# Kernel tuning notes

Measured on AMD Instinct MI355X. Metric: run time of the kernel, lower is better.

The kernel has to match this reference:

```python
import jax, jax.numpy as jnp
import numpy as np

NUM_HEADS = 8
SCALES = (1, 2, 4)
EPS = 1e-06


def _linear_attention(q, k, v, scale):
    # q: [B,h,Nq,d], k,v: [B,h,N,d]; all float32 (matches .float() in torch)
    q = jax.nn.elu(q * scale) + 1.0
    k = jax.nn.elu(k * scale) + 1.0
    kv = jnp.einsum('bhnd,bhne->bhde', k, v)          # [B,h,d,d]
    o = jnp.einsum('bhnd,bhde->bhne', q, kv)          # [B,h,Nq,d]
    k_sum = k.sum(axis=2)                              # [B,h,d]
    norm = jnp.einsum('bhnd,bhd->bhn', q, k_sum)[..., None]
    norm = jnp.maximum(norm, EPS)
    return o / norm


def setup_inputs() -> dict:
    key = jax.random.key(0)
    k1, k2, k3 = jax.random.split(key, 3)
    B, C, H, W = 4, 256, 128, 128
    x = jax.random.normal(k1, (B, C, H, W), dtype=jnp.float32)
    W_qkv = jax.random.normal(k2, (3 * C, C), dtype=jnp.float32) * 0.02
    W_proj = jax.random.normal(k3, (C, C), dtype=jnp.float32) * 0.02
    scale_weights = jnp.ones((len(SCALES),), dtype=jnp.float32) / len(SCALES)
    return {'x': x, 'W_qkv': W_qkv, 'W_proj': W_proj, 'scale_weights': scale_weights}


def reference(x, W_qkv, W_proj, scale_weights):
    B, C, H, W = x.shape
    h = NUM_HEADS
    d = C // h
    N = H * W
    scale = d ** (-0.5)

    # 1x1 conv == channel matmul
    qkv = jnp.einsum('bchw,oc->bohw', x, W_qkv)        # [B,3C,H,W]
    qkv = qkv.reshape(B, 3, h, d, N)
    qkv = jnp.transpose(qkv, (1, 0, 2, 4, 3))          # [3,B,h,N,d]
    q, k, v = qkv[0], qkv[1], qkv[2]

    sw = jax.nn.softmax(scale_weights)
    out = sw[0] * _linear_attention(q, k, v, scale)    # [B,h,N,d]

    for i, s in enumerate(SCALES[1:], 1):
        pH, pW = max(1, H // s), max(1, W // s)
        # adaptive avg pool with divisible sizes == block mean
        qg = q.reshape(B, h, H, W, d)
        qp = qg.reshape(B, h, pH, s, pW, s, d).mean(axis=(3, 5))  # [B,h,pH,pW,d]
        qp = qp.reshape(B, h, pH * pW, d)
        ao = _linear_attention(qp, k, v, scale).reshape(B, h, pH, pW, d)
        # bilinear, align_corners=False (half-pixel) == jax 'linear'
        ao = jax.image.resize(ao, (B, h, H, W, d), method='linear')
        out = out + sw[i] * ao.reshape(B, h, N, d)

    # [B,h,N,d] -> [B,N,C] -> [B,C,H,W]
    out = jnp.transpose(out, (0, 2, 1, 3)).reshape(B, N, C)
    out = jnp.transpose(out, (0, 2, 1)).reshape(B, C, H, W)
    out = jnp.einsum('bchw,oc->bohw', out, W_proj)
    return out
```

## Files before the change

### kernel.cpp

```cpp
#include <hip/hip_runtime.h>
#include <cstdint>
#include <cstddef>

#define GN 16384
#define QK_SCALE 0.17677669529663687f

typedef __attribute__((ext_vector_type(8))) __bf16 bf16x8;
typedef __attribute__((ext_vector_type(4))) float f32x4;
typedef __attribute__((ext_vector_type(8))) unsigned short us8;
typedef __attribute__((ext_vector_type(4))) unsigned short us4;

__device__ __forceinline__ float qk_act(float z) {
  return z > 0.0f ? z + 1.0f : __expf(z);
}

__device__ __forceinline__ unsigned short f2bf_rn(float v) {
  union { float f; unsigned u; } a; a.f = v;
  unsigned u = a.u;
  unsigned r = u + 0x7fffu + ((u >> 16) & 1u);
  return (unsigned short)(r >> 16);
}
__device__ __forceinline__ float bf2f(unsigned short h) {
  union { unsigned u; float f; } a; a.u = ((unsigned)h) << 16; return a.f;
}

#define GLLDS(SRC, DST) __builtin_amdgcn_global_load_lds( \
    (const __attribute__((address_space(1))) void*)(SRC), \
    (__attribute__((address_space(3))) void*)(DST), 16, 0, 0)

__global__ __launch_bounds__(256) void split_w(
    const float* __restrict__ in, unsigned short* __restrict__ h,
    unsigned short* __restrict__ l, int n4)
{
  int i = blockIdx.x * 256 + threadIdx.x;
  if (i >= n4) return;
  float4 v = ((const float4*)in)[i];
  us4 vh, vl;
  vh[0] = f2bf_rn(v.x); vl[0] = f2bf_rn(v.x - bf2f(vh[0]));
  vh[1] = f2bf_rn(v.y); vl[1] = f2bf_rn(v.y - bf2f(vh[1]));
  vh[2] = f2bf_rn(v.z); vl[2] = f2bf_rn(v.z - bf2f(vh[2]));
  vh[3] = f2bf_rn(v.w); vl[3] = f2bf_rn(v.w - bf2f(vh[3]));
  ((us4*)h)[i] = vh;
  ((us4*)l)[i] = vl;
}

__global__ __launch_bounds__(256) void split_x_t(
    const float* __restrict__ xb, unsigned short* __restrict__ xh,
    unsigned short* __restrict__ xl)
{
  __shared__ float ts[32][65];
  const int t  = threadIdx.x;
  const int n0 = blockIdx.x * 64;
  const int c0 = blockIdx.y * 32;
  const int z  = blockIdx.z;
  const float* src0 = xb + (size_t)z * 256 * GN;
  unsigned short* xho = xh + (size_t)z * GN * 256;
  unsigned short* xlo = xl + (size_t)z * GN * 256;
  {
    const int c  = t >> 3;
    const int nc = (t & 7) * 8;
    const float* src = src0 + ((size_t)(c0 + c)) * GN + n0 + nc;
    float4 v0 = *(const float4*)src;
    float4 v1 = *(const float4*)(src + 4);
    ts[c][nc + 0] = v0.x; ts[c][nc + 1] = v0.y; ts[c][nc + 2] = v0.z; ts[c][nc + 3] = v0.w;
    ts[c][nc + 4] = v1.x; ts[c][nc + 5] = v1.y; ts[c][nc + 6] = v1.z; ts[c][nc + 7] = v1.w;
  }
  __syncthreads();
  {
    const int n  = t & 63;
    const int cg = (t >> 6) * 8;
    us8 vh, vl;
#pragma unroll
    for (int j = 0; j < 8; ++j) {
      float v = ts[cg + j][n];
      unsigned short hh = f2bf_rn(v);
      vh[j] = hh;
      vl[j] = f2bf_rn(v - bf2f(hh));
    }
    size_t off = ((size_t)(n0 + n)) * 256 + c0 + cg;
    *(us8*)(xho + off) = vh;
    *(us8*)(xlo + off) = vl;
  }
}

template<int M, bool KACT, bool HEADMAJ>
__global__ __launch_bounds__(256) void gemm_mfma(
    const unsigned short* __restrict__ Wh, const unsigned short* __restrict__ Wl,
    const unsigned short* __restrict__ Xh, const unsigned short* __restrict__ Xl,
    float* __restrict__ Out, size_t XBS)
{
  constexpr int MT = M / 128;
  __shared__ __align__(16) char lds[32768];
  const int tid = threadIdx.x;
  const int w = tid >> 6;
  const int l = tid & 63;

  const int per  = gridDim.x >> 3;
  const int bid  = blockIdx.x;
  const int lbid = (bid & 7) * per + (bid >> 3);
  const int mt = lbid % MT;
  const int nt = (lbid / MT) & 127;
  const int b  = lbid / (MT * 128);

  const int m0 = mt * 128;
  const int n0 = nt * 128;

  const unsigned short* xh_b = Xh + (size_t)b * XBS;
  const unsigned short* xl_b = Xl + (size_t)b * XBS;

  f32x4 acc[4][4];
  const f32x4 zz = {0.f, 0.f, 0.f, 0.f};
#pragma unroll
  for (int i = 0; i < 4; ++i)
#pragma unroll
    for (int j = 0; j < 4; ++j) acc[i][j] = zz;

  const int wm = w >> 1, wn = w & 1;
  const int lr = l & 15, lk = l >> 4;
  const int ra  = wm * 64 + lr;
  const int rb  = wn * 64 + lr;
  const int cxa = (lk ^ (lr & 3)) << 4;

  for (int kt = 0; kt < 256; kt += 32) {
#pragma unroll
    for (int j = 0; j < 2; ++j) {
      const int r0 = w * 32 + j * 16;
      const int r  = r0 + (l >> 2);
      const int lc = (((l & 3) ^ (r & 3)) << 3);
      const size_t wrow = (size_t)(m0 + r) * 256 + kt + lc;
      const size_t xrow = HEADMAJ
          ? (size_t)(kt >> 5) * ((size_t)GN * 32) + (size_t)(n0 + r) * 32 + lc
          : (size_t)(n0 + r) * 256 + kt + lc;
      GLLDS(Wh + wrow,   lds + 0     + r0 * 64);
      GLLDS(Wl + wrow,   lds + 8192  + r0 * 64);
      GLLDS(xh_b + xrow, lds + 16384 + r0 * 64);
      GLLDS(xl_b + xrow, lds + 24576 + r0 * 64);
    }
    __syncthreads();

    bf16x8 ah[4], al[4], bh[4], bl[4];
#pragma unroll
    for (int s = 0; s < 4; ++s) {
      const int oa = (ra + s * 16) * 64 + cxa;
      const int ob = (rb + s * 16) * 64 + cxa;
      ah[s] = *(const bf16x8*)(lds + 0     + oa);
      al[s] = *(const bf16x8*)(lds + 8192  + oa);
      bh[s] = *(const bf16x8*)(lds + 16384 + ob);
      bl[s] = *(const bf16x8*)(lds + 24576 + ob);
    }
#pragma unroll
    for (int ms = 0; ms < 4; ++ms)
#pragma unroll
      for (int ns = 0; ns < 4; ++ns) {
        acc[ms][ns] = __builtin_amdgcn_mfma_f32_16x16x32_bf16(ah[ms], bh[ns], acc[ms][ns], 0, 0, 0);
        acc[ms][ns] = __builtin_amdgcn_mfma_f32_16x16x32_bf16(ah[ms], bl[ns], acc[ms][ns], 0, 0, 0);
        acc[ms][ns] = __builtin_amdgcn_mfma_f32_16x16x32_bf16(al[ms], bh[ns], acc[ms][ns], 0, 0, 0);
      }
    __syncthreads();
  }

  const bool act = KACT && (m0 >= 256 && m0 < 512);
#pragma unroll
  for (int ms = 0; ms < 4; ++ms)
#pragma unroll
    for (int ns = 0; ns < 4; ++ns) {
      const int m = m0 + wm * 64 + ms * 16 + lk * 4;
      const int n = n0 + wn * 64 + ns * 16 + lr;
      float* op = Out + ((size_t)b * M + m) * GN + n;
#pragma unroll
      for (int r = 0; r < 4; ++r) {
        float v = acc[ms][ns][r];
        if (act) v = qk_act(v * QK_SCALE);
        op[(size_t)r * GN] = v;
      }
    }
}

__global__ __launch_bounds__(256) void kv_ksum(
    const float* __restrict__ qkv, float* __restrict__ part)
{
  __shared__ __align__(16) float ksh[32][68];
  __shared__ __align__(16) float vsh[32][68];
  const int tid = threadIdx.x;
  const int bh = blockIdx.y;
  const int b = bh >> 3;
  const int head = bh & 7;
  const int dd = tid & 31;
  const int eg = tid >> 5;

  const float* Kb = qkv + ((size_t)b * 768 + 256 + head * 32) * GN;
  const float* Vb = qkv + ((size_t)b * 768 + 512 + head * 32) * GN;
  const int pbase = blockIdx.x * 256;

  float acc[4] = {0.f, 0.f, 0.f, 0.f};
  float ksacc = 0.f;

  for (int st = 0; st < 256; st += 64) {
    const int p0 = pbase + st;
#pragma unroll
    for (int t = 0; t < 2; ++t) {
      int idx = t * 256 + tid;
      int ch = idx >> 4;
      int c4 = idx & 15;
      *(float4*)&ksh[ch][c4 * 4] = *(const float4*)(Kb + (size_t)ch * GN + p0 + c4 * 4);
      *(float4*)&vsh[ch][c4 * 4] = *(const float4*)(Vb + (size_t)ch * GN + p0 + c4 * 4);
    }
    __syncthreads();
#pragma unroll
    for (int pg = 0; pg < 16; ++pg) {
      float4 kd = *(const float4*)&ksh[dd][pg * 4];
#pragma unroll
      for (int j = 0; j < 4; ++j) {
        float4 vv = *(const float4*)&vsh[eg * 4 + j][pg * 4];
        acc[j] += kd.x * vv.x + kd.y * vv.y + kd.z * vv.z + kd.w * vv.w;
      }
      if (eg == 0) ksacc += kd.x + kd.y + kd.z + kd.w;
    }
    __syncthreads();
  }

  float* pp = part + ((size_t)blockIdx.x * 32 + bh) * 1056;
  float4 av = {acc[0], acc[1], acc[2], acc[3]};
  *(float4*)(pp + dd * 32 + eg * 4) = av;
  if (eg == 0) pp[1024 + dd] = ksacc;
}

__global__ __launch_bounds__(256) void kv_reduce(
    const float* __restrict__ part, float* __restrict__ kvbuf,
    float* __restrict__ ksumbuf)
{
  const int g = blockIdx.x * 256 + threadIdx.x;
  const int bh = g / 1056;
  const int idx = g - bh * 1056;
  float s = 0.f;
#pragma unroll 4
  for (int c = 0; c < 64; ++c) s += part[((size_t)c * 32 + bh) * 1056 + idx];
  if (idx < 1024) kvbuf[bh * 1024 + idx] = s;
  else            ksumbuf[bh * 32 + (idx - 1024)] = s;
}

__global__ __launch_bounds__(256) void pool_q(
    const float* __restrict__ qkv, float* __restrict__ qp2,
    float* __restrict__ qp4)
{
  const int g = blockIdx.x * 256 + threadIdx.x;
  const int x4 = g & 31;
  const int y4 = (g >> 5) & 31;
  const int bc = g >> 10;
  const int b = bc >> 8;
  const int c = bc & 255;
  const float* src = qkv + ((size_t)b * 768 + c) * GN + (y4 * 4) * 128 + x4 * 4;
  float4 r0 = *(const float4*)(src);
  float4 r1 = *(const float4*)(src + 128);
  float4 r2 = *(const float4*)(src + 256);
  float4 r3 = *(const float4*)(src + 384);
  float m00 = (r0.x + r0.y + r1.x + r1.y) * 0.25f;
  float m01 = (r0.z + r0.w + r1.z + r1.w) * 0.25f;
  float m10 = (r2.x + r2.y + r3.x + r3.y) * 0.25f;
  float m11 = (r2.z + r2.w + r3.z + r3.w) * 0.25f;
  float m4 = (m00 + m01 + m10 + m11) * 0.25f;
  float* p2 = qp2 + (size_t)bc * 4096 + (y4 * 2) * 64 + x4 * 2;
  float2 wa = {m00, m01};
  float2 wb = {m10, m11};
  *(float2*)p2 = wa;
  *(float2*)(p2 + 64) = wb;
  qp4[(size_t)bc * 1024 + y4 * 32 + x4] = m4;
}

__global__ __launch_bounds__(256) void pooled_attn(
    float* qp, const float* __restrict__ kvbuf,
    const float* __restrict__ ksumbuf, int Np)
{
  __shared__ __align__(16) float kv_s[32][32];
  __shared__ float ks_s[32];
  const int tid = threadIdx.x;
  const int bh = blockIdx.y;
  const int b = bh >> 3;
  const int head = bh & 7;
  const int p = blockIdx.x * 256 + tid;

  const float* kvb = kvbuf + (size_t)bh * 1024;
#pragma unroll
  for (int t = 0; t < 4; ++t) ((float*)kv_s)[t * 256 + tid] = kvb[t * 256 + tid];
  if (tid < 32) ks_s[tid] = ksumbuf[bh * 32 + tid];
  __syncthreads();

  float* q0 = qp + ((size_t)(b * 256 + head * 32)) * Np + p;
  float qa[32];
#pragma unroll
  for (int dd = 0; dd < 32; ++dd) qa[dd] = qk_act(q0[(size_t)dd * Np] * QK_SCALE);

  float o1[32];
#pragma unroll
  for (int e = 0; e < 32; ++e) o1[e] = 0.f;
  float norm = 0.f;
#pragma unroll
  for (int dd = 0; dd < 32; ++dd) {
    float qv = qa[dd];
    norm += qv * ks_s[dd];
#pragma unroll
    for (int e4 = 0; e4 < 8; ++e4) {
      float4 kvv = *(const float4*)&kv_s[dd][e4 * 4];
      o1[e4 * 4 + 0] += qv * kvv.x;
      o1[e4 * 4 + 1] += qv * kvv.y;
      o1[e4 * 4 + 2] += qv * kvv.z;
      o1[e4 * 4 + 3] += qv * kvv.w;
    }
  }
  norm = fmaxf(norm, 1e-6f);
  float inv1 = 1.0f / norm;
#pragma unroll
  for (int e = 0; e < 32; ++e) q0[(size_t)e * Np] = o1[e] * inv1;
}

__global__ __launch_bounds__(512) void fused_out(
    const float* __restrict__ qkv, const float* __restrict__ kvbuf,
    const float* __restrict__ ksumbuf, const float* __restrict__ ao2,
    const float* __restrict__ ao4, const float* __restrict__ swin,
    unsigned short* __restrict__ preh, unsigned short* __restrict__ prel,
    size_t PBS)
{
  __shared__ __align__(16) float kv_s[32][32];
  __shared__ float ks_s[32];
  __shared__ __align__(16) float a2_s[4][32][64];
  __shared__ __align__(16) float a4_s[3][32][32];
  const int tid = threadIdx.x;
  const int m2 = blockIdx.x;
  const int bh = blockIdx.y;
  const int b = bh >> 3;
  const int head = bh & 7;
  const int n = m2 * 512 + tid;

  const float* kvb = kvbuf + (size_t)bh * 1024;
#pragma unroll
  for (int t = 0; t < 2; ++t) ((float*)kv_s)[t * 512 + tid] = kvb[t * 512 + tid];
  if (tid < 32) ks_s[tid] = ksumbuf[bh * 32 + tid];

  const float* a2 = ao2 + ((size_t)(b * 256 + head * 32)) * 4096;
  const float* a4 = ao4 + ((size_t)(b * 256 + head * 32)) * 1024;
  int r2[4], r4[3];
#pragma unroll
  for (int j = 0; j < 4; ++j) {
    int a = 2 * m2 - 1 + j; r2[j] = a < 0 ? 0 : (a > 63 ? 63 : a);
  }
#pragma unroll
  for (int j = 0; j < 3; ++j) {
    int c = m2 - 1 + j; r4[j] = c < 0 ? 0 : (c > 31 ? 31 : c);
  }
#pragma unroll
  for (int t = 0; t < 4; ++t) {
    int fidx = t * 512 + tid;
    int x4 = fidx & 15, e = (fidx >> 4) & 31, j = fidx >> 9;
    *(float4*)&a2_s[j][e][x4 * 4] =
        *(const float4*)(a2 + (size_t)e * 4096 + r2[j] * 64 + x4 * 4);
  }
#pragma unroll
  for (int t = 0; t < 2; ++t) {
    int fidx = t * 512 + tid;
    if (fidx < 768) {
      int x4 = fidx & 7, e = (fidx >> 3) & 31, j = fidx >> 8;
      *(float4*)&a4_s[j][e][x4 * 4] =
          *(const float4*)(a4 + (size_t)e * 1024 + r4[j] * 32 + x4 * 4);
    }
  }
  __syncthreads();

  float s0 = swin[0], s1 = swin[1], s2 = swin[2];
  float mx = fmaxf(s0, fmaxf(s1, s2));
  float ex0 = __expf(s0 - mx), ex1 = __expf(s1 - mx), ex2 = __expf(s2 - mx);
  float sinv = 1.0f / (ex0 + ex1 + ex2);
  float sw0 = ex0 * sinv, sw1 = ex1 * sinv, sw2 = ex2 * sinv;

  const float* q0 = qkv + ((size_t)b * 768 + head * 32) * GN + n;
  float qa[32];
#pragma unroll
  for (int dd = 0; dd < 32; ++dd) qa[dd] = qk_act(q0[(size_t)dd * GN] * QK_SCALE);

  float o1[32];
#pragma unroll
  for (int e = 0; e < 32; ++e) o1[e] = 0.f;
  float norm = 0.f;
#pragma unroll
  for (int dd = 0; dd < 32; ++dd) {
    float qv = qa[dd];
    norm += qv * ks_s[dd];
#pragma unroll
    for (int e4 = 0; e4 < 8; ++e4) {
      float4 kvv = *(const float4*)&kv_s[dd][e4 * 4];
      o1[e4 * 4 + 0] += qv * kvv.x;
      o1[e4 * 4 + 1] += qv * kvv.y;
      o1[e4 * 4 + 2] += qv * kvv.z;
      o1[e4 * 4 + 3] += qv * kvv.w;
    }
  }
  norm = fmaxf(norm, 1e-6f);
  float inv1 = 1.0f / norm;

  const int mm = tid >> 8;
  const int yb = (tid >> 7) & 1;
  const int x  = n & 127;
  const int lj2 = mm + yb;
  const float wy2 = yb ? 0.25f : 0.75f;
  const int xu = x >> 1;
  const int x20 = xu - 1 + (x & 1);
  const float wx2 = (x & 1) ? 0.25f : 0.75f;
  const int x20c = x20 < 0 ? 0 : x20;
  const int x21c = (x20 + 1) < 63 ? (x20 + 1) : 63;
  const int lj4 = mm;
  const float wy4 = (0.625f - 0.5f * (float)mm) + 0.25f * (float)yb;
  const int xq = x >> 2, xr = x & 3;
  const int x40 = xq - 1 + (xr >> 1);
  const float wx4 = ((xr & 1) ? 0.875f : 0.625f) - ((xr >> 1) ? 0.5f : 0.0f);
  const int x40c = x40 < 0 ? 0 : x40;
  const int x41c = (x40 + 1) < 31 ? (x40 + 1) : 31;

  const float wy2i = 1.f - wy2, wx2i = 1.f - wx2;
  const float wy4i = 1.f - wy4, wx4i = 1.f - wx4;

  unsigned short* ph = preh + (size_t)b * PBS + (size_t)head * (GN * 32) + (size_t)n * 32;
  unsigned short* pl = prel + (size_t)b * PBS + (size_t)head * (GN * 32) + (size_t)n * 32;

#pragma unroll
  for (int t4 = 0; t4 < 4; ++t4) {
    us8 vh, vl;
#pragma unroll
    for (int j = 0; j < 8; ++j) {
      const int e = t4 * 8 + j;
      float u2 = wy2i * (wx2i * a2_s[lj2][e][x20c] + wx2 * a2_s[lj2][e][x21c])
               + wy2  * (wx2i * a2_s[lj2 + 1][e][x20c] + wx2 * a2_s[lj2 + 1][e][x21c]);
      float u4 = wy4i * (wx4i * a4_s[lj4][e][x40c] + wx4 * a4_s[lj4][e][x41c])
               + wy4  * (wx4i * a4_s[lj4 + 1][e][x40c] + wx4 * a4_s[lj4 + 1][e][x41c]);
      float val = sw0 * o1[e] * inv1 + sw1 * u2 + sw2 * u4;
      unsigned short hh = f2bf_rn(val);
      vh[j] = hh;
      vl[j] = f2bf_rn(val - bf2f(hh));
    }
    *(us8*)(ph + t4 * 8) = vh;
    *(us8*)(pl + t4 * 8) = vl;
  }
}

extern "C" void kernel_launch(void* const* d_in, const int* in_sizes, int n_in,
                              void* d_out, int out_size, void* d_ws, size_t ws_size,
                              hipStream_t stream) {
  const float* x     = (const float*)d_in[0];
  const float* Wqkv  = (const float*)d_in[1];
  const float* Wproj = (const float*)d_in[2];
  const float* swin  = (const float*)d_in[3];
  float* out = (float*)d_out;
  float* ws  = (float*)d_ws;

  float* qkv = ws;
  float* xtreg = ws + (size_t)50331648;
  unsigned short* xt_h = (unsigned short*)xtreg;
  unsigned short* xt_l = xt_h + (size_t)8388608;
  float* qp2 = xtreg;
  float* qp4 = xtreg + (size_t)4194304;
  float* part = xtreg + (size_t)5242880;
  float* kvb  = xtreg + (size_t)8388608;
  float* ksum = kvb + 32768;
  unsigned short* wh1 = (unsigned short*)(ksum + 1024);
  unsigned short* wl1 = wh1 + 196608;
  unsigned short* wh2 = wl1 + 196608;
  unsigned short* wl2 = wh2 + 65536;
  unsigned short* preh = (unsigned short*)qkv + (size_t)1024 * GN;
  unsigned short* prel = (unsigned short*)qkv + (size_t)1280 * GN;
  const size_t PBS = (size_t)1536 * GN;

  dim3 blk(256);
  split_w<<<dim3(192), blk, 0, stream>>>(Wqkv, wh1, wl1, 49152);
  split_w<<<dim3(64),  blk, 0, stream>>>(Wproj, wh2, wl2, 16384);
  for (int g = 0; g < 2; ++g) {
    split_x_t<<<dim3(256, 8, 2), blk, 0, stream>>>(
        x + (size_t)g * 2 * 256 * GN, xt_h, xt_l);
    gemm_mfma<768, true, false><<<dim3(1536), blk, 0, stream>>>(
        wh1, wl1, xt_h, xt_l, qkv + (size_t)g * 2 * 768 * GN, (size_t)GN * 256);
  }
  kv_ksum<<<dim3(64, 32), blk, 0, stream>>>(qkv, part);
  kv_reduce<<<dim3(132), blk, 0, stream>>>(part, kvb, ksum);
  pool_q<<<dim3(4096), blk, 0, stream>>>(qkv, qp2, qp4);
  pooled_attn<<<dim3(16, 32), blk, 0, stream>>>(qp2, kvb, ksum, 4096);
  pooled_attn<<<dim3(4, 32), blk, 0, stream>>>(qp4, kvb, ksum, 1024);
  fused_out<<<dim3(32, 32), dim3(512), 0, stream>>>(qkv, kvb, ksum, qp2, qp4, swin,
                                                    preh, prel, PBS);
  gemm_mfma<256, false, true><<<dim3(1024), blk, 0, stream>>>(wh2, wl2, preh, prel, out, PBS);
}
```

Measured before the change: 399.8 us.

## Enlarge GEMM block tile to 256x128 with 512 threads to share X tile

The split-bf16 MFMA GEMM now uses 8 waves per block and a 256-row M tile instead of 128, so each staged X tile (high and low parts) is reused across twice as many weight rows. The load loop is reorganised to distribute 48 16-row groups across the 8 waves, and LDS grows to 48KB. Grid sizes for both GEMMs are halved. This cuts redundant global loads of the activation tile, at the cost of higher LDS use per block and fewer blocks, which may lower occupancy.

```diff
diff --git a/kernel.cpp b/kernel.cpp
--- a/kernel.cpp
+++ b/kernel.cpp
@@ -84,13 +84,13 @@
 }
 
 template<int M, bool KACT, bool HEADMAJ>
-__global__ __launch_bounds__(256) void gemm_mfma(
+__global__ __launch_bounds__(512) void gemm_mfma(
     const unsigned short* __restrict__ Wh, const unsigned short* __restrict__ Wl,
     const unsigned short* __restrict__ Xh, const unsigned short* __restrict__ Xl,
     float* __restrict__ Out, size_t XBS)
 {
-  constexpr int MT = M / 128;
-  __shared__ __align__(16) char lds[32768];
+  constexpr int MT = M / 256;
+  __shared__ __align__(16) char lds[49152];
   const int tid = threadIdx.x;
   const int w = tid >> 6;
   const int l = tid & 63;
@@ -102,7 +102,7 @@
   const int nt = (lbid / MT) & 127;
   const int b  = lbid / (MT * 128);
 
-  const int m0 = mt * 128;
+  const int m0 = mt * 256;
   const int n0 = nt * 128;
 
   const unsigned short* xh_b = Xh + (size_t)b * XBS;
@@ -123,18 +123,26 @@
 
   for (int kt = 0; kt < 256; kt += 32) {
 #pragma unroll
-    for (int j = 0; j < 2; ++j) {
-      const int r0 = w * 32 + j * 16;
-      const int r  = r0 + (l >> 2);
-      const int lc = (((l & 3) ^ (r & 3)) << 3);
-      const size_t wrow = (size_t)(m0 + r) * 256 + kt + lc;
-      const size_t xrow = HEADMAJ
-          ? (size_t)(kt >> 5) * ((size_t)GN * 32) + (size_t)(n0 + r) * 32 + lc
-          : (size_t)(n0 + r) * 256 + kt + lc;
-      GLLDS(Wh + wrow,   lds + 0     + r0 * 64);
-      GLLDS(Wl + wrow,   lds + 8192  + r0 * 64);
-      GLLDS(xh_b + xrow, lds + 16384 + r0 * 64);
-      GLLDS(xl_b + xrow, lds + 24576 + r0 * 64);
+    for (int j = 0; j < 6; ++j) {
+      const int gidx = w * 6 + j;
+      int g, sel;
+      if (gidx < 16)      { sel = 0; g = gidx; }
+      else if (gidx < 32) { sel = 1; g = gidx - 16; }
+      else if (gidx < 40) { sel = 2; g = gidx - 32; }
+      else                { sel = 3; g = gidx - 40; }
+      const int rl = g * 16 + (l >> 2);
+      const int lc = (((l & 3) ^ (rl & 3)) << 3);
+      char* dst = lds + (sel == 0 ? 0 : sel == 1 ? 16384 : sel == 2 ? 32768 : 40960)
+                      + g * 1024;
+      if (sel <= 1) {
+        const size_t wrow = (size_t)(m0 + rl) * 256 + kt + lc;
+        GLLDS((sel == 0 ? Wh : Wl) + wrow, dst);
+      } else {
+        const size_t xrow = HEADMAJ
+            ? (size_t)(kt >> 5) * ((size_t)GN * 32) + (size_t)(n0 + rl) * 32 + lc
+            : (size_t)(n0 + rl) * 256 + kt + lc;
+        GLLDS((sel == 2 ? xh_b : xl_b) + xrow, dst);
+      }
     }
     __syncthreads();
 
@@ -144,9 +152,9 @@
       const int oa = (ra + s * 16) * 64 + cxa;
       const int ob = (rb + s * 16) * 64 + cxa;
       ah[s] = *(const bf16x8*)(lds + 0     + oa);
-      al[s] = *(const bf16x8*)(lds + 8192  + oa);
-      bh[s] = *(const bf16x8*)(lds + 16384 + ob);
-      bl[s] = *(const bf16x8*)(lds + 24576 + ob);
+      al[s] = *(const bf16x8*)(lds + 16384 + oa);
+      bh[s] = *(const bf16x8*)(lds + 32768 + ob);
+      bl[s] = *(const bf16x8*)(lds + 40960 + ob);
     }
 #pragma unroll
     for (int ms = 0; ms < 4; ++ms)
@@ -473,7 +481,7 @@
   for (int g = 0; g < 2; ++g) {
     split_x_t<<<dim3(256, 8, 2), blk, 0, stream>>>(
         x + (size_t)g * 2 * 256 * GN, xt_h, xt_l);
-    gemm_mfma<768, true, false><<<dim3(1536), blk, 0, stream>>>(
+    gemm_mfma<768, true, false><<<dim3(768), dim3(512), 0, stream>>>(
         wh1, wl1, xt_h, xt_l, qkv + (size_t)g * 2 * 768 * GN, (size_t)GN * 256);
   }
   kv_ksum<<<dim3(64, 32), blk, 0, stream>>>(qkv, part);
@@ -483,5 +491,5 @@
   pooled_attn<<<dim3(4, 32), blk, 0, stream>>>(qp4, kvb, ksum, 1024);
   fused_out<<<dim3(32, 32), dim3(512), 0, stream>>>(qkv, kvb, ksum, qp2, qp4, swin,
                                                     preh, prel, PBS);
-  gemm_mfma<256, false, true><<<dim3(1024), blk, 0, stream>>>(wh2, wl2, preh, prel, out, PBS);
-}
+  gemm_mfma<256, false, true><<<dim3(512), dim3(512), 0, stream>>>(wh2, wl2, preh, prel, out, PBS);
+}
```

Measured after the change: 423.7 us. 6.0% more time.
